# Kernel optimization log

Hardware: AMD Instinct MI355X
Metric: run time of the kernel (lower is better)

Reference implementation:

```python
import jax, jax.numpy as jnp
import numpy as np
import math

N = 100000
E = 1600000
IN_DIM = 64
OUT_DIM = 64
EPS = 1e-5


def setup_inputs() -> dict:
    key = jax.random.key(0)
    ks = jax.random.split(key, 12)
    s = 1.0 / math.sqrt(IN_DIM)
    inp = {
        "geo_x": jax.random.normal(ks[0], (N, IN_DIM), dtype=jnp.float32),
        "euc_x": jax.random.normal(ks[1], (N, IN_DIM), dtype=jnp.float32),
        "Wq": jax.random.uniform(ks[2], (OUT_DIM, IN_DIM), minval=-s, maxval=s, dtype=jnp.float32),
        "bq": jnp.zeros((OUT_DIM,), jnp.float32),
        "Wk": jax.random.uniform(ks[3], (OUT_DIM, IN_DIM), minval=-s, maxval=s, dtype=jnp.float32),
        "bk": jnp.zeros((OUT_DIM,), jnp.float32),
        "Wv": jax.random.uniform(ks[4], (OUT_DIM, IN_DIM), minval=-s, maxval=s, dtype=jnp.float32),
        "bv": jnp.zeros((OUT_DIM,), jnp.float32),
        "Wskip": jax.random.uniform(ks[5], (OUT_DIM, IN_DIM), minval=-s, maxval=s, dtype=jnp.float32),
        "bskip": jnp.zeros((OUT_DIM,), jnp.float32),
        "ln_w": jnp.ones((OUT_DIM,), jnp.float32),
        "ln_b": jnp.zeros((OUT_DIM,), jnp.float32),
        "edge_index": jax.random.randint(ks[6], (2, E), 0, N, dtype=jnp.int64),
    }
    return inp


def reference(geo_x, euc_x, Wq, bq, Wk, bk, Wv, bv, Wskip, bskip, ln_w, ln_b, edge_index):
    n = euc_x.shape[0]
    src, dst = edge_index[0], edge_index[1]

    # TransformerConv, heads=1: q from target (euc), k/v from source (geo)
    q = euc_x @ Wq.T + bq                      # [N, C]
    k = geo_x @ Wk.T + bk                      # [N, C]
    v = geo_x @ Wv.T + bv                      # [N, C]
    C = q.shape[-1]

    # per-edge attention logits
    alpha = jnp.sum(q[dst] * k[src], axis=-1) / math.sqrt(C)   # [E]

    # segment softmax over incoming edges of each destination node
    amax = jax.ops.segment_max(alpha, dst, num_segments=n)
    amax = jnp.where(jnp.isfinite(amax), amax, 0.0)
    ex = jnp.exp(alpha - amax[dst])
    denom = jax.ops.segment_sum(ex, dst, num_segments=n)
    w = ex / (denom[dst] + 1e-16)                              # [E]

    # scatter-aggregate weighted values + root (skip) transform
    agg = jax.ops.segment_sum(w[:, None] * v[src], dst, num_segments=n)  # [N, C]
    out = agg + euc_x @ Wskip.T + bskip

    # PyG LayerNorm, mode='graph', batch=None: normalize over all nodes+channels
    mean = out.mean()
    xc = out - mean
    std = jnp.sqrt(jnp.mean(xc * xc))
    out = xc / (std + EPS) * ln_w + ln_b

    return jax.nn.relu(out)
```

## Files before the change

kernel.cpp:

```cpp
#include <hip/hip_runtime.h>
#include <hip/hip_fp16.h>


using short8 = __attribute__((ext_vector_type(8))) short;
using f32x4  = __attribute__((ext_vector_type(4))) float;
using h2     = __attribute__((ext_vector_type(2))) _Float16;

#define QSCALE 31.75f
#define VDESC  0.031496062992f
#define SCI    1.7889250e-4f

#define CAP   4608
#define NCBMAX 400

__device__ inline unsigned short f2bf(float f) {
    unsigned u = __float_as_uint(f);
    unsigned r = u + 0x7FFFu + ((u >> 16) & 1u);
    return (unsigned short)(r >> 16);
}
__device__ inline unsigned short f2h(float f) {
    union { _Float16 h; unsigned short u; } c;
    c.h = (_Float16)f;
    return c.u;
}
__device__ inline h2 u2h2(unsigned u) {
    union { unsigned u; h2 h; } c; c.u = u; return c.h;
}
__device__ inline signed char f2i8(float f) {
    float v = f * QSCALE;
    v = fminf(fmaxf(v, -127.f), 127.f);
    return (signed char)__float2int_rn(v);
}

__device__ inline float fexp2(float x) {
#if __has_builtin(__builtin_amdgcn_exp2f)
    return __builtin_amdgcn_exp2f(x);
#else
    return __expf(x * 0.6931471805599453f);
#endif
}

__device__ inline int dot8i(uint2 q, uint2 k) {
#if __has_builtin(__builtin_amdgcn_sdot4)
    int t = __builtin_amdgcn_sdot4((int)q.x, (int)k.x, 0, false);
    return  __builtin_amdgcn_sdot4((int)q.y, (int)k.y, t, false);
#else
    int t = 0;
    #pragma unroll
    for (int i = 0; i < 4; ++i) {
        int qa = (int)(q.x << (24 - 8 * i)) >> 24;
        int ka = (int)(k.x << (24 - 8 * i)) >> 24;
        int qb = (int)(q.y << (24 - 8 * i)) >> 24;
        int kb = (int)(k.y << (24 - 8 * i)) >> 24;
        t += qa * ka + qb * kb;
    }
    return t;
#endif
}

__global__ __launch_bounds__(256) void k0_wconv(
    const float* __restrict__ Wq, const float* __restrict__ Wk,
    const float* __restrict__ Wv, const float* __restrict__ Wsk,
    unsigned short* __restrict__ wbf, int* __restrict__ zbase, int zcount)
{
    if (blockIdx.x == 16) {
        for (int i = threadIdx.x; i < zcount; i += 256) zbase[i] = 0;
        return;
    }
    int mat = blockIdx.x >> 2;
    int i4  = (blockIdx.x & 3) * 256 + threadIdx.x;
    const float* W = (mat == 0) ? Wq : (mat == 1) ? Wk : (mat == 2) ? Wv : Wsk;
    float4 w = *(const float4*)(W + (long)i4 * 4);
    ushort4 o;
    o.x = f2bf(w.x); o.y = f2bf(w.y); o.z = f2bf(w.z); o.w = f2bf(w.w);
    *(ushort4*)(wbf + (long)mat * 4096 + (long)i4 * 4) = o;
}

__global__ __launch_bounds__(256) void k1_proj(
    const float* __restrict__ geo, const float* __restrict__ euc,
    const unsigned short* __restrict__ wbf,
    const float* __restrict__ bq, const float* __restrict__ bk,
    const float* __restrict__ bv, const float* __restrict__ bsk,
    signed char* __restrict__ q8b, signed char* __restrict__ kv8,
    unsigned short* __restrict__ skb, int N)
{
    __shared__ __align__(16) char smem[2 * 64 * 208];
    const int tid  = threadIdx.x;
    const int lane = tid & 63;
    const int w    = tid >> 6;
    const int qq   = lane >> 4;
    const int m    = lane & 15;
    const long base = (long)blockIdx.x * 64;
    const long node = base + w * 16 + m;
    const bool valid = (node < N);

    float4 fe[2][2], fg[2][2];
    {
        const float* pe = euc + node * 64;
        const float* pg = geo + node * 64;
        #pragma unroll
        for (int kh = 0; kh < 2; ++kh) {
            int off = kh * 32 + qq * 8;
            if (valid) {
                fe[kh][0] = *(const float4*)(pe + off);
                fe[kh][1] = *(const float4*)(pe + off + 4);
                fg[kh][0] = *(const float4*)(pg + off);
                fg[kh][1] = *(const float4*)(pg + off + 4);
            } else {
                fe[kh][0] = fe[kh][1] = fg[kh][0] = fg[kh][1] =
                    make_float4(0.f, 0.f, 0.f, 0.f);
            }
        }
    }
    auto cvt = [](float4 a, float4 b) -> short8 {
        short8 r;
        r[0] = (short)f2bf(a.x); r[1] = (short)f2bf(a.y);
        r[2] = (short)f2bf(a.z); r[3] = (short)f2bf(a.w);
        r[4] = (short)f2bf(b.x); r[5] = (short)f2bf(b.y);
        r[6] = (short)f2bf(b.z); r[7] = (short)f2bf(b.w);
        return r;
    };
    short8 ae[2], ag[2];
    #pragma unroll
    for (int kh = 0; kh < 2; ++kh) {
        ae[kh] = cvt(fe[kh][0], fe[kh][1]);
        ag[kh] = cvt(fg[kh][0], fg[kh][1]);
    }

    auto do_mat = [&](const short8 a[2], int mat, f32x4 acc[4]) {
        #pragma unroll
        for (int kh = 0; kh < 2; ++kh) {
            #pragma unroll
            for (int nt = 0; nt < 4; ++nt) {
                short8 bf = *(const short8*)(wbf + (long)mat * 4096 +
                                             (nt * 16 + m) * 64 + kh * 32 + qq * 8);
                acc[nt] = __builtin_amdgcn_mfma_f32_16x16x32_bf16(a[kh], bf, acc[nt], 0, 0, 0);
            }
        }
    };

    auto emit_i8 = [&](const f32x4 acc[4], const float* __restrict__ bias,
                       char* tile, int off) {
        #pragma unroll
        for (int nt = 0; nt < 4; ++nt) {
            int c = nt * 16 + m;
            float bs = bias[c];
            #pragma unroll
            for (int r = 0; r < 4; ++r) {
                int nl = w * 16 + qq * 4 + r;
                *(signed char*)(tile + nl * 208 + off + c) = f2i8(acc[nt][r] + bs);
            }
        }
    };
    auto emit_h = [&](const f32x4 acc[4], const float* __restrict__ bias,
                      char* tile, int off) {
        #pragma unroll
        for (int nt = 0; nt < 4; ++nt) {
            int c = nt * 16 + m;
            float bs = bias[c];
            #pragma unroll
            for (int r = 0; r < 4; ++r) {
                int nl = w * 16 + qq * 4 + r;
                *(unsigned short*)(tile + nl * 208 + off + c * 2) = f2h(acc[nt][r] + bs);
            }
        }
    };

    char* tile0 = smem;
    char* tile1 = smem + 64 * 208;
    {
        f32x4 acc[4];
        #pragma unroll
        for (int nt = 0; nt < 4; ++nt) acc[nt] = (f32x4)(0.f);
        do_mat(ae, 0, acc);
        emit_i8(acc, bq, tile0, 0);
        #pragma unroll
        for (int nt = 0; nt < 4; ++nt) acc[nt] = (f32x4)(0.f);
        do_mat(ae, 3, acc);
        emit_h(acc, bsk, tile0, 64);
        #pragma unroll
        for (int nt = 0; nt < 4; ++nt) acc[nt] = (f32x4)(0.f);
        do_mat(ag, 1, acc);
        emit_i8(acc, bk, tile1, 0);
        #pragma unroll
        for (int nt = 0; nt < 4; ++nt) acc[nt] = (f32x4)(0.f);
        do_mat(ag, 2, acc);
        emit_i8(acc, bv, tile1, 64);
    }
    __syncthreads();

    {
        int n = tid >> 2, j = tid & 3;
        long nd = base + n;
        if (nd < N)
            *(int4*)(q8b + nd * 64 + j * 16) = *(const int4*)(tile0 + n * 208 + j * 16);
    }
    #pragma unroll
    for (int it = 0; it < 2; ++it) {
        int idx = it * 256 + tid;
        int n = idx >> 3, j = idx & 7;
        long nd = base + n;
        if (nd < N)
            *(int4*)((char*)skb + nd * 128 + j * 16) =
                *(const int4*)(tile0 + n * 208 + 64 + j * 16);
    }
    #pragma unroll
    for (int it = 0; it < 2; ++it) {
        int idx = it * 256 + tid;
        int n = idx >> 3, j = idx & 7;
        long nd = base + n;
        if (nd < N)
            *(int4*)(kv8 + nd * 128 + j * 16) = *(const int4*)(tile1 + n * 208 + j * 16);
    }
}

__global__ __launch_bounds__(512) void k2a_part(
    const int* __restrict__ ei, int E, int N,
    int* __restrict__ ccur, unsigned* __restrict__ tmp)
{
    __shared__ unsigned ebuf[4096];
    __shared__ unsigned short cbuf[4096];
    __shared__ int h[NCBMAX], offA[NCBMAX], lc[NCBMAX], creg[NCBMAX];
    __shared__ int sc[512];

    const int tid = threadIdx.x;
    const int NCB = (N + 255) >> 8;
    const long e0 = (long)blockIdx.x * 4096;
    const int tileN = (int)(((long)E - e0 < 4096) ? ((long)E - e0) : 4096);

    for (int i = tid; i < NCB; i += 512) { h[i] = 0; lc[i] = 0; }
    __syncthreads();

    const int* srcp = ei;
    const int* dstp = ei + E;
    unsigned wj[8];
    int cbj[8];
    #pragma unroll
    for (int j = 0; j < 8; ++j) {
        int i = j * 512 + tid;
        wj[j] = 0u; cbj[j] = -1;
        if (i < tileN) {
            int d = dstp[e0 + i], s = srcp[e0 + i];
            cbj[j] = d >> 8;
            wj[j]  = ((unsigned)(d & 255) << 17) | (unsigned)s;
            atomicAdd(&h[cbj[j]], 1);
        }
    }
    __syncthreads();

    sc[tid] = (tid < NCB) ? h[tid] : 0;
    __syncthreads();
    int own = sc[tid];
    for (int off = 1; off < 512; off <<= 1) {
        int v = (tid >= off) ? sc[tid - off] : 0;
        __syncthreads();
        sc[tid] += v;
        __syncthreads();
    }
    if (tid < NCB) offA[tid] = sc[tid] - own;
    if (tid < NCB && h[tid] > 0)
        creg[tid] = atomicAdd(&ccur[tid], h[tid]);
    __syncthreads();

    #pragma unroll
    for (int j = 0; j < 8; ++j) {
        if (cbj[j] >= 0) {
            int pos = offA[cbj[j]] + atomicAdd(&lc[cbj[j]], 1);
            ebuf[pos] = wj[j];
            cbuf[pos] = (unsigned short)cbj[j];
        }
    }
    __syncthreads();

    #pragma unroll
    for (int j = 0; j < 8; ++j) {
        int i = j * 512 + tid;
        if (i < tileN) {
            int cb = cbuf[i];
            int r  = creg[cb] + (i - offA[cb]);
            if (r < CAP) tmp[(long)cb * CAP + r] = ebuf[i];
        }
    }
}

__global__ __launch_bounds__(512, 8) void k3_attn(
    const signed char* __restrict__ q8b, const signed char* __restrict__ kv8,
    const unsigned short* __restrict__ skb,
    const int* __restrict__ ccnt, const unsigned* __restrict__ tmp,
    float* __restrict__ out, float* __restrict__ partS, float* __restrict__ partSS,
    int N)
{
    __shared__ unsigned bkt[64 * 65];
    __shared__ int dcnt[64];
    __shared__ unsigned char perm[64];
    __shared__ float redS[8], redSS[8];
    const int tid  = threadIdx.x;
    const int lane = tid & 63;
    const int w    = tid >> 6;
    const int g0   = tid >> 3;
    const int gl   = tid & 7;
    const int bin  = blockIdx.x;
    const int cb   = bin >> 2;
    const unsigned sub = (unsigned)(bin & 3);
    const long nodeBase = (long)bin * 64;

    if (tid < 64) dcnt[tid] = 0;
    __syncthreads();

    int len = ccnt[cb];
    if (len > CAP) len = CAP;
    const unsigned* reg = tmp + (long)cb * CAP;
    for (int e = tid; e < len; e += 512) {
        unsigned wv = reg[e];
        if (((wv >> 23) & 3u) == sub) {
            int d = (wv >> 17) & 63;
            int slot = atomicAdd(&dcnt[d], 1);
            if (slot < 64) bkt[d * 65 + slot] = wv & 0x1FFFFu;
        }
    }
    __syncthreads();

    if (tid < 64) {
        int d = dcnt[tid]; if (d > 64) d = 64;
        int r = 0;
        for (int j = 0; j < 64; ++j) {
            int dj = dcnt[j]; if (dj > 64) dj = 64;
            r += (dj > d) || ((dj == d) && (j < tid));
        }
        perm[r] = (unsigned char)tid;
    }
    __syncthreads();

    const int row  = perm[g0];
    const long node = nodeBase + row;

    uint2 qu = make_uint2(0, 0);
    if (node < N) qu = *(const uint2*)(q8b + node * 64 + gl * 8);

    int deg = dcnt[row];
    if (deg > 64) deg = 64;

    float den = 0.f;
    float a0=0.f,a1=0.f,a2=0.f,a3=0.f,a4=0.f,a5=0.f,a6=0.f,a7=0.f;

    auto vacc = [&](uint2 v, float ex) {
        a0 = fmaf((float)((int)(v.x << 24) >> 24), ex, a0);
        a1 = fmaf((float)((int)(v.x << 16) >> 24), ex, a1);
        a2 = fmaf((float)((int)(v.x <<  8) >> 24), ex, a2);
        a3 = fmaf((float)((int)(v.x      ) >> 24), ex, a3);
        a4 = fmaf((float)((int)(v.y << 24) >> 24), ex, a4);
        a5 = fmaf((float)((int)(v.y << 16) >> 24), ex, a5);
        a6 = fmaf((float)((int)(v.y <<  8) >> 24), ex, a6);
        a7 = fmaf((float)((int)(v.y      ) >> 24), ex, a7);
    };

    if (deg > 0) {
        const int rb  = row * 65;
        const int dm1 = deg - 1;
        unsigned sA = bkt[rb];
        const signed char* pA = kv8 + (long)sA * 128 + gl * 8;
        uint2 kA = *(const uint2*)pA;
        uint2 vA = *(const uint2*)(pA + 64);

        for (int s = 0; s < deg; s += 2) {
            int i1 = (s + 1 < deg) ? s + 1 : dm1;
            unsigned sB = bkt[rb + i1];
            const signed char* pB = kv8 + (long)sB * 128 + gl * 8;
            uint2 kB = *(const uint2*)pB;
            uint2 vB = *(const uint2*)(pB + 64);

            int t0 = dot8i(qu, kA);
            t0 += __shfl_xor(t0, 1);
            t0 += __shfl_xor(t0, 2);
            t0 += __shfl_xor(t0, 4);
            float ex0 = fexp2((float)t0 * SCI);
            den += ex0;
            vacc(vA, ex0);

            int i2 = (s + 2 < deg) ? s + 2 : dm1;
            unsigned sC = bkt[rb + i2];
            const signed char* pC = kv8 + (long)sC * 128 + gl * 8;
            kA = *(const uint2*)pC;
            vA = *(const uint2*)(pC + 64);

            int t1 = dot8i(qu, kB);
            t1 += __shfl_xor(t1, 1);
            t1 += __shfl_xor(t1, 2);
            t1 += __shfl_xor(t1, 4);
            float ex1 = (s + 1 < deg) ? fexp2((float)t1 * SCI) : 0.f;
            den += ex1;
            vacc(vB, ex1);
        }
    }

    float sacc = 0.f, ssacc = 0.f;
    if (node < N) {
        float inv = VDESC / (den + 1e-16f);
        uint4 sk = *(const uint4*)((const char*)skb + node * 128 + gl * 16);
        h2 s0 = u2h2(sk.x), s1 = u2h2(sk.y), s2 = u2h2(sk.z), s3 = u2h2(sk.w);
        float o0 = a0 * inv + (float)s0.x, o1 = a1 * inv + (float)s0.y;
        float o2 = a2 * inv + (float)s1.x, o3 = a3 * inv + (float)s1.y;
        float o4 = a4 * inv + (float)s2.x, o5 = a5 * inv + (float)s2.y;
        float o6 = a6 * inv + (float)s3.x, o7 = a7 * inv + (float)s3.y;
        *(float4*)(out + node * 64 + gl * 8)     = make_float4(o0, o1, o2, o3);
        *(float4*)(out + node * 64 + gl * 8 + 4) = make_float4(o4, o5, o6, o7);
        sacc  = (o0 + o1 + o2 + o3) + (o4 + o5 + o6 + o7);
        ssacc = o0*o0 + o1*o1 + o2*o2 + o3*o3 + o4*o4 + o5*o5 + o6*o6 + o7*o7;
    }
    #pragma unroll
    for (int m = 1; m <= 32; m <<= 1) {
        sacc  += __shfl_xor(sacc, m);
        ssacc += __shfl_xor(ssacc, m);
    }
    if (lane == 0) { redS[w] = sacc; redSS[w] = ssacc; }
    __syncthreads();
    if (tid == 0) {
        float s = 0.f, ss = 0.f;
        #pragma unroll
        for (int i = 0; i < 8; ++i) { s += redS[i]; ss += redSS[i]; }
        partS[bin]  = s;
        partSS[bin] = ss;
    }
}

__global__ __launch_bounds__(256) void k35_stats(
    const float* __restrict__ partS, const float* __restrict__ partSS,
    int nparts, float* __restrict__ stats, float M)
{
    __shared__ float rs[256], rss[256];
    float s = 0.f, ss = 0.f;
    for (int i = threadIdx.x; i < nparts; i += 256) { s += partS[i]; ss += partSS[i]; }
    rs[threadIdx.x] = s; rss[threadIdx.x] = ss;
    __syncthreads();
    for (int st = 128; st > 0; st >>= 1) {
        if (threadIdx.x < st) {
            rs[threadIdx.x]  += rs[threadIdx.x + st];
            rss[threadIdx.x] += rss[threadIdx.x + st];
        }
        __syncthreads();
    }
    if (threadIdx.x == 0) {
        float mean = rs[0] / M;
        float var  = rss[0] / M - mean * mean;
        if (var < 0.f) var = 0.f;
        stats[0] = mean;
        stats[1] = 1.f / (sqrtf(var) + 1e-5f);
    }
}

__global__ __launch_bounds__(256) void k4_ln(
    float* __restrict__ out, const float* __restrict__ lnw,
    const float* __restrict__ lnb, const float* __restrict__ stats, int M4)
{
    int i = blockIdx.x * 256 + threadIdx.x;
    if (i >= M4) return;
    float mean = stats[0], scale = stats[1];
    float4 x = *(float4*)(out + (long)i * 4);
    int c4 = (i & 15) * 4;
    float4 wv = *(const float4*)(lnw + c4);
    float4 bv = *(const float4*)(lnb + c4);
    x.x = fmaxf((x.x - mean) * scale * wv.x + bv.x, 0.f);
    x.y = fmaxf((x.y - mean) * scale * wv.y + bv.y, 0.f);
    x.z = fmaxf((x.z - mean) * scale * wv.z + bv.z, 0.f);
    x.w = fmaxf((x.w - mean) * scale * wv.w + bv.w, 0.f);
    *(float4*)(out + (long)i * 4) = x;
}

extern "C" void kernel_launch(void* const* d_in, const int* in_sizes, int n_in,
                              void* d_out, int out_size, void* d_ws, size_t ws_size,
                              hipStream_t stream)
{
    const float* geo = (const float*)d_in[0];
    const float* euc = (const float*)d_in[1];
    const float* Wq  = (const float*)d_in[2];
    const float* bq  = (const float*)d_in[3];
    const float* Wk  = (const float*)d_in[4];
    const float* bk  = (const float*)d_in[5];
    const float* Wv  = (const float*)d_in[6];
    const float* bv  = (const float*)d_in[7];
    const float* Wsk = (const float*)d_in[8];
    const float* bsk = (const float*)d_in[9];
    const float* lnw = (const float*)d_in[10];
    const float* lnb = (const float*)d_in[11];
    const int*   ei  = (const int*)d_in[12];

    const int N = in_sizes[0] / 64;
    const int E = in_sizes[12] / 2;
    const int K = (N + 63) / 64;
    const int NCB = (N + 255) >> 8;
    float* out = (float*)d_out;

    char* p = (char*)d_ws;
    signed char*    q8b   = (signed char*)p;    p += (size_t)N * 64;
    signed char*    kv8   = (signed char*)p;    p += (size_t)N * 128;
    unsigned short* skb   = (unsigned short*)p; p += (size_t)N * 64 * 2;
    unsigned*       tmp   = (unsigned*)p;       p += (size_t)NCB * CAP * 4;
    unsigned short* wbf   = (unsigned short*)p; p += (size_t)4 * 4096 * 2;
    int* ccur = (int*)p;  p += (size_t)(NCB + 8) * 4;
    float* partS  = (float*)p; p += (size_t)K * 4;
    float* partSS = (float*)p; p += (size_t)K * 4;
    float* stats  = (float*)p;

    const int PB = (N + 63) / 64;

    k0_wconv<<<17, 256, 0, stream>>>(Wq, Wk, Wv, Wsk, wbf, ccur, NCB + 8);
    k1_proj<<<PB, 256, 0, stream>>>(geo, euc, wbf, bq, bk, bv, bsk,
                                    q8b, kv8, skb, N);
    const int GA = (E + 4095) / 4096;
    k2a_part<<<GA, 512, 0, stream>>>(ei, E, N, ccur, tmp);
    k3_attn<<<K, 512, 0, stream>>>(q8b, kv8, skb, ccur, tmp, out, partS, partSS, N);
    k35_stats<<<1, 256, 0, stream>>>(partS, partSS, K, stats, (float)N * 64.0f);
    const int M4 = N * 16;
    k4_ln<<<(M4 + 255) / 256, 256, 0, stream>>>(out, lnw, lnb, stats, M4);
}
```

Measured before the change: 217.2 us.

## Interleave K/V int8 per 8-channel group and process 128 nodes per projection block

The k/v int8 layout is changed so each 8-channel k chunk sits next to its 8-channel v chunk. The attention gather can then fetch both with one 16-byte load per edge instead of two 8-byte loads. The projection kernel now handles 128 nodes per block, reusing weight fragments loaded into registers for two node tiles, and uses launch bounds with 3 blocks per CU. This raises register and shared memory use in the projection kernel in exchange for fewer global weight loads and fewer gather transactions.

```diff
diff --git a/kernel.cpp b/kernel.cpp
--- a/kernel.cpp
+++ b/kernel.cpp
@@ -76,7 +76,7 @@
     *(ushort4*)(wbf + (long)mat * 4096 + (long)i4 * 4) = o;
 }
 
-__global__ __launch_bounds__(256) void k1_proj(
+__global__ __launch_bounds__(256, 3) void k1_proj(
     const float* __restrict__ geo, const float* __restrict__ euc,
     const unsigned short* __restrict__ wbf,
     const float* __restrict__ bq, const float* __restrict__ bk,
@@ -84,63 +84,58 @@
     signed char* __restrict__ q8b, signed char* __restrict__ kv8,
     unsigned short* __restrict__ skb, int N)
 {
-    __shared__ __align__(16) char smem[2 * 64 * 208];
+    __shared__ __align__(16) char smem[4 * 64 * 208];
     const int tid  = threadIdx.x;
     const int lane = tid & 63;
     const int w    = tid >> 6;
     const int qq   = lane >> 4;
     const int m    = lane & 15;
-    const long base = (long)blockIdx.x * 64;
-    const long node = base + w * 16 + m;
-    const bool valid = (node < N);
-
-    float4 fe[2][2], fg[2][2];
-    {
-        const float* pe = euc + node * 64;
-        const float* pg = geo + node * 64;
+    const long base = (long)blockIdx.x * 128;
+
+    char* te0 = smem;
+    char* te1 = smem + 64 * 208;
+    char* tg0 = smem + 2 * 64 * 208;
+    char* tg1 = smem + 3 * 64 * 208;
+
+    const long nodeA0 = base + w * 16 + m;
+    const long nodeA1 = base + 64 + w * 16 + m;
+
+    auto loadA = [&](const float* __restrict__ x, long node, short8 a[2]) {
+        const float* px = x + node * 64;
+        const bool v = (node < N);
         #pragma unroll
         for (int kh = 0; kh < 2; ++kh) {
-            int off = kh * 32 + qq * 8;
-            if (valid) {
-                fe[kh][0] = *(const float4*)(pe + off);
-                fe[kh][1] = *(const float4*)(pe + off + 4);
-                fg[kh][0] = *(const float4*)(pg + off);
-                fg[kh][1] = *(const float4*)(pg + off + 4);
-            } else {
-                fe[kh][0] = fe[kh][1] = fg[kh][0] = fg[kh][1] =
-                    make_float4(0.f, 0.f, 0.f, 0.f);
-            }
-        }
-    }
-    auto cvt = [](float4 a, float4 b) -> short8 {
-        short8 r;
-        r[0] = (short)f2bf(a.x); r[1] = (short)f2bf(a.y);
-        r[2] = (short)f2bf(a.z); r[3] = (short)f2bf(a.w);
-        r[4] = (short)f2bf(b.x); r[5] = (short)f2bf(b.y);
-        r[6] = (short)f2bf(b.z); r[7] = (short)f2bf(b.w);
-        return r;
-    };
-    short8 ae[2], ag[2];
-    #pragma unroll
-    for (int kh = 0; kh < 2; ++kh) {
-        ae[kh] = cvt(fe[kh][0], fe[kh][1]);
-        ag[kh] = cvt(fg[kh][0], fg[kh][1]);
-    }
-
-    auto do_mat = [&](const short8 a[2], int mat, f32x4 acc[4]) {
-        #pragma unroll
-        for (int kh = 0; kh < 2; ++kh) {
+            float4 f0 = v ? *(const float4*)(px + kh * 32 + qq * 8)
+                          : make_float4(0.f, 0.f, 0.f, 0.f);
+            float4 f1 = v ? *(const float4*)(px + kh * 32 + qq * 8 + 4)
+                          : make_float4(0.f, 0.f, 0.f, 0.f);
+            short8 r;
+            r[0] = (short)f2bf(f0.x); r[1] = (short)f2bf(f0.y);
+            r[2] = (short)f2bf(f0.z); r[3] = (short)f2bf(f0.w);
+            r[4] = (short)f2bf(f1.x); r[5] = (short)f2bf(f1.y);
+            r[6] = (short)f2bf(f1.z); r[7] = (short)f2bf(f1.w);
+            a[kh] = r;
+        }
+    };
+    auto loadB = [&](int mat, short8 b[2][4]) {
+        #pragma unroll
+        for (int kh = 0; kh < 2; ++kh)
             #pragma unroll
-            for (int nt = 0; nt < 4; ++nt) {
-                short8 bf = *(const short8*)(wbf + (long)mat * 4096 +
+            for (int nt = 0; nt < 4; ++nt)
+                b[kh][nt] = *(const short8*)(wbf + (long)mat * 4096 +
                                              (nt * 16 + m) * 64 + kh * 32 + qq * 8);
-                acc[nt] = __builtin_amdgcn_mfma_f32_16x16x32_bf16(a[kh], bf, acc[nt], 0, 0, 0);
-            }
-        }
-    };
-
-    auto emit_i8 = [&](const f32x4 acc[4], const float* __restrict__ bias,
-                       char* tile, int off) {
+    };
+    auto mmul = [&](const short8 a[2], const short8 b[2][4], f32x4 acc[4]) {
+        #pragma unroll
+        for (int nt = 0; nt < 4; ++nt) acc[nt] = (f32x4)(0.f);
+        #pragma unroll
+        for (int kh = 0; kh < 2; ++kh)
+            #pragma unroll
+            for (int nt = 0; nt < 4; ++nt)
+                acc[nt] = __builtin_amdgcn_mfma_f32_16x16x32_bf16(a[kh], b[kh][nt], acc[nt], 0, 0, 0);
+    };
+
+    auto emit_i8 = [&](const f32x4 acc[4], const float* __restrict__ bias, char* tile) {
         #pragma unroll
         for (int nt = 0; nt < 4; ++nt) {
             int c = nt * 16 + m;
@@ -148,12 +143,11 @@
             #pragma unroll
             for (int r = 0; r < 4; ++r) {
                 int nl = w * 16 + qq * 4 + r;
-                *(signed char*)(tile + nl * 208 + off + c) = f2i8(acc[nt][r] + bs);
+                *(signed char*)(tile + nl * 208 + c) = f2i8(acc[nt][r] + bs);
             }
         }
     };
-    auto emit_h = [&](const f32x4 acc[4], const float* __restrict__ bias,
-                      char* tile, int off) {
+    auto emit_h = [&](const f32x4 acc[4], const float* __restrict__ bias, char* tile) {
         #pragma unroll
         for (int nt = 0; nt < 4; ++nt) {
             int c = nt * 16 + m;
@@ -161,56 +155,76 @@
             #pragma unroll
             for (int r = 0; r < 4; ++r) {
                 int nl = w * 16 + qq * 4 + r;
-                *(unsigned short*)(tile + nl * 208 + off + c * 2) = f2h(acc[nt][r] + bs);
+                *(unsigned short*)(tile + nl * 208 + 64 + c * 2) = f2h(acc[nt][r] + bs);
             }
         }
     };
-
-    char* tile0 = smem;
-    char* tile1 = smem + 64 * 208;
-    {
-        f32x4 acc[4];
-        #pragma unroll
-        for (int nt = 0; nt < 4; ++nt) acc[nt] = (f32x4)(0.f);
-        do_mat(ae, 0, acc);
-        emit_i8(acc, bq, tile0, 0);
-        #pragma unroll
-        for (int nt = 0; nt < 4; ++nt) acc[nt] = (f32x4)(0.f);
-        do_mat(ae, 3, acc);
-        emit_h(acc, bsk, tile0, 64);
-        #pragma unroll
-        for (int nt = 0; nt < 4; ++nt) acc[nt] = (f32x4)(0.f);
-        do_mat(ag, 1, acc);
-        emit_i8(acc, bk, tile1, 0);
-        #pragma unroll
-        for (int nt = 0; nt < 4; ++nt) acc[nt] = (f32x4)(0.f);
-        do_mat(ag, 2, acc);
-        emit_i8(acc, bv, tile1, 64);
-    }
-    __syncthreads();
-
-    {
-        int n = tid >> 2, j = tid & 3;
-        long nd = base + n;
-        if (nd < N)
-            *(int4*)(q8b + nd * 64 + j * 16) = *(const int4*)(tile0 + n * 208 + j * 16);
-    }
+    auto emit_kv = [&](const f32x4 acc[4], const float* __restrict__ bias,
+                       char* tile, int vpart) {
+        #pragma unroll
+        for (int nt = 0; nt < 4; ++nt) {
+            int c = nt * 16 + m;
+            float bs = bias[c];
+            int boff = (c >> 3) * 16 + vpart * 8 + (c & 7);
+            #pragma unroll
+            for (int r = 0; r < 4; ++r) {
+                int nl = w * 16 + qq * 4 + r;
+                *(signed char*)(tile + nl * 208 + boff) = f2i8(acc[nt][r] + bs);
+            }
+        }
+    };
+
+    short8 a0[2], a1[2];
+    short8 B0[2][4], B1[2][4];
+    f32x4 acc[4];
+
+    loadA(euc, nodeA0, a0);
+    loadA(euc, nodeA1, a1);
+    loadB(0, B0);
+    loadB(3, B1);
+    mmul(a0, B0, acc); emit_i8(acc, bq, te0);
+    mmul(a1, B0, acc); emit_i8(acc, bq, te1);
+    mmul(a0, B1, acc); emit_h(acc, bsk, te0);
+    mmul(a1, B1, acc); emit_h(acc, bsk, te1);
+
+    loadA(geo, nodeA0, a0);
+    loadA(geo, nodeA1, a1);
+    loadB(1, B0);
+    loadB(2, B1);
+    mmul(a0, B0, acc); emit_kv(acc, bk, tg0, 0);
+    mmul(a1, B0, acc); emit_kv(acc, bk, tg1, 0);
+    mmul(a0, B1, acc); emit_kv(acc, bv, tg0, 1);
+    mmul(a1, B1, acc); emit_kv(acc, bv, tg1, 1);
+    __syncthreads();
+
     #pragma unroll
-    for (int it = 0; it < 2; ++it) {
-        int idx = it * 256 + tid;
-        int n = idx >> 3, j = idx & 7;
-        long nd = base + n;
-        if (nd < N)
-            *(int4*)((char*)skb + nd * 128 + j * 16) =
-                *(const int4*)(tile0 + n * 208 + 64 + j * 16);
-    }
-    #pragma unroll
-    for (int it = 0; it < 2; ++it) {
-        int idx = it * 256 + tid;
-        int n = idx >> 3, j = idx & 7;
-        long nd = base + n;
-        if (nd < N)
-            *(int4*)(kv8 + nd * 128 + j * 16) = *(const int4*)(tile1 + n * 208 + j * 16);
+    for (int t = 0; t < 2; ++t) {
+        const char* te = t ? te1 : te0;
+        const char* tg = t ? tg1 : tg0;
+        const long tb = base + t * 64;
+        {
+            int n = tid >> 2, j = tid & 3;
+            long nd = tb + n;
+            if (nd < N)
+                *(int4*)(q8b + nd * 64 + j * 16) = *(const int4*)(te + n * 208 + j * 16);
+        }
+        #pragma unroll
+        for (int it = 0; it < 2; ++it) {
+            int idx = it * 256 + tid;
+            int n = idx >> 3, j = idx & 7;
+            long nd = tb + n;
+            if (nd < N)
+                *(int4*)((char*)skb + nd * 128 + j * 16) =
+                    *(const int4*)(te + n * 208 + 64 + j * 16);
+        }
+        #pragma unroll
+        for (int it = 0; it < 2; ++it) {
+            int idx = it * 256 + tid;
+            int n = idx >> 3, j = idx & 7;
+            long nd = tb + n;
+            if (nd < N)
+                *(int4*)(kv8 + nd * 128 + j * 16) = *(const int4*)(tg + n * 208 + j * 16);
+        }
     }
 }
 
@@ -343,53 +357,47 @@
     float den = 0.f;
     float a0=0.f,a1=0.f,a2=0.f,a3=0.f,a4=0.f,a5=0.f,a6=0.f,a7=0.f;
 
-    auto vacc = [&](uint2 v, float ex) {
-        a0 = fmaf((float)((int)(v.x << 24) >> 24), ex, a0);
-        a1 = fmaf((float)((int)(v.x << 16) >> 24), ex, a1);
-        a2 = fmaf((float)((int)(v.x <<  8) >> 24), ex, a2);
-        a3 = fmaf((float)((int)(v.x      ) >> 24), ex, a3);
-        a4 = fmaf((float)((int)(v.y << 24) >> 24), ex, a4);
-        a5 = fmaf((float)((int)(v.y << 16) >> 24), ex, a5);
-        a6 = fmaf((float)((int)(v.y <<  8) >> 24), ex, a6);
-        a7 = fmaf((float)((int)(v.y      ) >> 24), ex, a7);
+    auto vacc = [&](unsigned vx, unsigned vy, float ex) {
+        a0 = fmaf((float)((int)(vx << 24) >> 24), ex, a0);
+        a1 = fmaf((float)((int)(vx << 16) >> 24), ex, a1);
+        a2 = fmaf((float)((int)(vx <<  8) >> 24), ex, a2);
+        a3 = fmaf((float)((int)(vx      ) >> 24), ex, a3);
+        a4 = fmaf((float)((int)(vy << 24) >> 24), ex, a4);
+        a5 = fmaf((float)((int)(vy << 16) >> 24), ex, a5);
+        a6 = fmaf((float)((int)(vy <<  8) >> 24), ex, a6);
+        a7 = fmaf((float)((int)(vy      ) >> 24), ex, a7);
     };
 
     if (deg > 0) {
         const int rb  = row * 65;
         const int dm1 = deg - 1;
         unsigned sA = bkt[rb];
-        const signed char* pA = kv8 + (long)sA * 128 + gl * 8;
-        uint2 kA = *(const uint2*)pA;
-        uint2 vA = *(const uint2*)(pA + 64);
+        uint4 rA = *(const uint4*)(kv8 + (long)sA * 128 + gl * 16);
 
         for (int s = 0; s < deg; s += 2) {
             int i1 = (s + 1 < deg) ? s + 1 : dm1;
             unsigned sB = bkt[rb + i1];
-            const signed char* pB = kv8 + (long)sB * 128 + gl * 8;
-            uint2 kB = *(const uint2*)pB;
-            uint2 vB = *(const uint2*)(pB + 64);
-
-            int t0 = dot8i(qu, kA);
+            uint4 rB = *(const uint4*)(kv8 + (long)sB * 128 + gl * 16);
+
+            int t0 = dot8i(qu, make_uint2(rA.x, rA.y));
             t0 += __shfl_xor(t0, 1);
             t0 += __shfl_xor(t0, 2);
             t0 += __shfl_xor(t0, 4);
             float ex0 = fexp2((float)t0 * SCI);
             den += ex0;
-            vacc(vA, ex0);
+            vacc(rA.z, rA.w, ex0);
 
             int i2 = (s + 2 < deg) ? s + 2 : dm1;
             unsigned sC = bkt[rb + i2];
-            const signed char* pC = kv8 + (long)sC * 128 + gl * 8;
-            kA = *(const uint2*)pC;
-            vA = *(const uint2*)(pC + 64);
-
-            int t1 = dot8i(qu, kB);
+            rA = *(const uint4*)(kv8 + (long)sC * 128 + gl * 16);
+
+            int t1 = dot8i(qu, make_uint2(rB.x, rB.y));
             t1 += __shfl_xor(t1, 1);
             t1 += __shfl_xor(t1, 2);
             t1 += __shfl_xor(t1, 4);
             float ex1 = (s + 1 < deg) ? fexp2((float)t1 * SCI) : 0.f;
             den += ex1;
-            vacc(vB, ex1);
+            vacc(rB.z, rB.w, ex1);
         }
     }
 
@@ -501,11 +509,11 @@
     float* partSS = (float*)p; p += (size_t)K * 4;
     float* stats  = (float*)p;
 
-    const int PB = (N + 63) / 64;
+    const int PB2 = (N + 127) / 128;
 
     k0_wconv<<<17, 256, 0, stream>>>(Wq, Wk, Wv, Wsk, wbf, ccur, NCB + 8);
-    k1_proj<<<PB, 256, 0, stream>>>(geo, euc, wbf, bq, bk, bv, bsk,
-                                    q8b, kv8, skb, N);
+    k1_proj<<<PB2, 256, 0, stream>>>(geo, euc, wbf, bq, bk, bv, bsk,
+                                     q8b, kv8, skb, N);
     const int GA = (E + 4095) / 4096;
     k2a_part<<<GA, 512, 0, stream>>>(ei, E, N, ccur, tmp);
     k3_attn<<<K, 512, 0, stream>>>(q8b, kv8, skb, ccur, tmp, out, partS, partSS, N);
```

Measured after the change: 212.1 us. 2.3% less time.
